# Kernel optimization log

Measured on AMD Instinct MI355X. Metric: run time of the kernel, lower is better.

Reference implementation:

```python
import jax, jax.numpy as jnp
import numpy as np

B, S, H, D, K = 262144, 120, 256, 64, 64  # batch, state_dim, vae_hidden_dim, latent_dim, n_codes


def _lin(k, i, o):
    return jax.random.normal(k, (i, o), jnp.float32) / np.sqrt(i).astype(np.float32)


def setup_inputs() -> dict:
    key = jax.random.key(0)
    ks = jax.random.split(key, 9)
    return {
        "inputs": jax.random.normal(ks[0], (B, S), jnp.float32),
        "enc_w1": _lin(ks[1], S, H), "enc_b1": jnp.zeros((H,), jnp.float32),
        "enc_w2": _lin(ks[2], H, H), "enc_b2": jnp.zeros((H,), jnp.float32),
        "enc_w3": _lin(ks[3], H, D), "enc_b3": jnp.zeros((D,), jnp.float32),
        "codebook": jax.random.uniform(ks[4], (K, D), jnp.float32),  # NearestEmbed weight (rand init)
        "fc3_w": _lin(ks[5], D, H), "fc3_b": jnp.zeros((H,), jnp.float32),
        "fc4_w": _lin(ks[6], H, H), "fc4_b": jnp.zeros((H,), jnp.float32),
        "fc5_w": _lin(ks[7], H, S), "fc5_b": jnp.zeros((S,), jnp.float32),
    }


def _nearest(z, codebook):
    # squared L2 distance via |z|^2 - 2 z.C^T + |c|^2; fused GEMM form
    d = ((z * z).sum(-1, keepdims=True)
         - 2.0 * (z @ codebook.T)
         + (codebook * codebook).sum(-1))  # [B, K]
    idx = jnp.argmin(d, axis=-1)  # [B]
    return codebook[idx], idx


def reference(inputs, enc_w1, enc_b1, enc_w2, enc_b2, enc_w3, enc_b3,
              codebook, fc3_w, fc3_b, fc4_w, fc4_b, fc5_w, fc5_b):
    # encode
    h = jax.nn.relu(inputs @ enc_w1 + enc_b1)
    h = jax.nn.relu(h @ enc_w2 + enc_b2)
    z_e = h @ enc_w3 + enc_b3  # [B, D]
    # emb(z_e, weight_sg=True): straight-through to input, codebook detached
    q, argmin = _nearest(z_e, jax.lax.stop_gradient(codebook))
    z_q = z_e + jax.lax.stop_gradient(q - z_e)
    # emb(z_e.detach()): grads flow only to codebook
    emb, _ = _nearest(jax.lax.stop_gradient(z_e), codebook)
    # decode (recon_type=1)
    r = jax.nn.relu(z_q @ fc3_w + fc3_b)
    r = jax.nn.relu(r @ fc4_w + fc4_b)
    s_hat = r @ fc5_w + fc5_b  # [B, S]
    return s_hat, z_e, emb, argmin
```

## Files before the change

kernel.cpp:

```cpp
#include <hip/hip_runtime.h>


#define B_TOTAL 262144
#define THR 0.02f

typedef float  f32x4 __attribute__((ext_vector_type(4)));
typedef short  s16x8 __attribute__((ext_vector_type(8)));

#define ZB ((size_t)B_TOTAL * 120)
#define EB ((size_t)B_TOTAL * 184)
#define AB ((size_t)B_TOTAL * 248)

#define WS_STAB   0
#define WS_CBT    30720
#define WS_CNORM  47104
#define WS_COUNT  47360
#define WS_LIST   47424
#define WS_PKW1   1096064
#define WS_PKW2   1227136
#define WS_PKE3   1489280
#define WS_PKW4   1554816
#define WS_CN2    1620352

static __device__ __forceinline__ unsigned short f2bf(float x) {
    unsigned int u = __float_as_uint(x);
    return (unsigned short)((u + 0x7fffu + ((u >> 16) & 1u)) >> 16);
}
static __device__ __forceinline__ void splitbf(float a, unsigned short& h, unsigned short& s) {
    unsigned hb = __float_as_uint(a) & 0xffff0000u;
    h = (unsigned short)(hb >> 16);
    s = f2bf(a - __uint_as_float(hb));
}
static __device__ __forceinline__ void splitbf_t(float a, unsigned short& h, unsigned short& s) {
    unsigned u = __float_as_uint(a);
    h = (unsigned short)(u >> 16);
    float d = a - __uint_as_float(u & 0xffff0000u);
    s = (unsigned short)(__float_as_uint(d) >> 16);
}
static __device__ __forceinline__ float sqnc(float v) {
    float s = v * v;
    asm volatile("" : "+v"(s));
    return s;
}
static __device__ __forceinline__ float np_sumsq64(const float* a) {
    float r8[8];
#pragma unroll
    for (int j = 0; j < 8; ++j) r8[j] = sqnc(a[j]);
#pragma unroll
    for (int i = 8; i < 64; i += 8)
#pragma unroll
        for (int j = 0; j < 8; ++j) r8[j] += sqnc(a[i + j]);
    return ((r8[0] + r8[1]) + (r8[2] + r8[3])) + ((r8[4] + r8[5]) + (r8[6] + r8[7]));
}

static __device__ __forceinline__ int swz(int row, int col) {
    return row * 256 + ((((col >> 3) ^ (row & 7))) << 3) + (col & 7);
}

__global__ __launch_bounds__(256)
void vq_prep(const float* __restrict__ cb,
             const float* __restrict__ dw3, const float* __restrict__ db3,
             const float* __restrict__ dw4, const float* __restrict__ db4,
             const float* __restrict__ dw5, const float* __restrict__ db5,
             float* __restrict__ s_tab, float* __restrict__ cbT, float* __restrict__ cnorm)
{
    __shared__ float c_row[64];
    __shared__ float u1[256];
    __shared__ float u2[256];
    const int k = blockIdx.x;
    const int t = threadIdx.x;

    if (t < 64) c_row[t] = cb[k * 64 + t];
    __syncthreads();
    {
        float s = 0.f;
        for (int f = 0; f < 64; ++f) s = fmaf(c_row[f], dw3[f * 256 + t], s);
        u1[t] = fmaxf(s + db3[t], 0.f);
    }
    if (t < 64) cbT[t * 64 + k] = c_row[t];
    if (t == 0) cnorm[k] = np_sumsq64(&cb[k * 64]);
    __syncthreads();
    {
        float s = 0.f;
        for (int f = 0; f < 256; ++f) s = fmaf(u1[f], dw4[f * 256 + t], s);
        u2[t] = fmaxf(s + db4[t], 0.f);
    }
    __syncthreads();
    if (t < 120) {
        float o = 0.f;
        for (int f = 0; f < 256; ++f) o = fmaf(u2[f], dw5[f * 120 + t], o);
        s_tab[k * 120 + t] = o + db5[t];
    }
}

__global__ __launch_bounds__(512)
void vq_pack(const float* __restrict__ w1, const float* __restrict__ w2,
             const float* __restrict__ ew3, const float* __restrict__ cb,
             const float* __restrict__ eb3,
             unsigned short* __restrict__ pw1, unsigned short* __restrict__ pw2,
             unsigned short* __restrict__ pe3, unsigned short* __restrict__ pw4,
             float* __restrict__ cn2, int* __restrict__ flag_count)
{
    const int t = threadIdx.x;
    int f = blockIdx.x;
    if (f == 0 && t == 0) *flag_count = 0;

    const int lane = t >> 3, j = t & 7;
    float a;
    unsigned short* dst;
    int nt, ks, KSN;

    if (f < 224) {
        const float* src; int srcK, ld;
        if (f < 64)       { src = w1;  dst = pw1; KSN = 4; nt = f >> 2;  ks = f & 3; srcK = 120; ld = 256; }
        else if (f < 192) { f -= 64;  src = w2;  dst = pw2; KSN = 8; nt = f >> 3; ks = f & 7; srcK = 256; ld = 256; }
        else              { f -= 192; src = ew3; dst = pe3; KSN = 8; nt = f >> 3; ks = f & 7; srcK = 256; ld = 64; }
        const int k = ks * 32 + (lane >> 4) * 8 + j;
        const int n = nt * 16 + (lane & 15);
        a = (k < srcK) ? src[k * ld + n] : 0.f;
    } else {
        int g = f - 224;
        dst = pw4; KSN = 8; nt = g >> 3; ks = g & 7;
        const int k = ks * 32 + (lane >> 4) * 8 + j;
        const int n = nt * 16 + (lane & 15);
        float s = 0.f;
        const float* er = ew3 + k * 64;
        const float* cr = cb + n * 64;
        for (int d = 0; d < 64; ++d) s = fmaf(er[d], cr[d], s);
        a = s;
        if (g == 0 && t < 64) {
            float ss = 0.f, e2 = 0.f;
            const float* c = cb + t * 64;
            for (int d = 0; d < 64; ++d) { ss = fmaf(c[d], c[d], ss); e2 = fmaf(eb3[d], c[d], e2); }
            cn2[t] = ss - 2.f * e2;
        }
    }

    unsigned short h, l;
    splitbf(a, h, l);
    const int base = (nt * KSN + ks) * 2 * 512;
    dst[base + t] = h;
    dst[base + 512 + t] = l;
}

__global__ __launch_bounds__(512, 4)
void vq_fast(const float* __restrict__ x,
             const float* __restrict__ b1, const float* __restrict__ b2,
             const float* __restrict__ eb3, const float* __restrict__ cb,
             const float* __restrict__ s_tab, const float* __restrict__ cn2,
             const unsigned short* __restrict__ pw1, const unsigned short* __restrict__ pw2,
             const unsigned short* __restrict__ pe3, const unsigned short* __restrict__ pw4,
             int* __restrict__ flag_count, int* __restrict__ flag_list,
             float* __restrict__ out)
{
    __shared__ __align__(16) unsigned char smem[32768];
    unsigned short* ph = (unsigned short*)smem;
    unsigned short* pl = (unsigned short*)(smem + 16384);
    float*          dm = (float*)smem;
    int*          idxs = (int*)(smem + 8704);

    const int t = threadIdx.x;
    const int w = t >> 6, l = t & 63;
    const int lr = l & 15;
    const int grow0 = blockIdx.x * 32;

    {
        const float* xb = x + (size_t)grow0 * 120;
        unsigned* ph32 = (unsigned*)ph;
        unsigned* pl32 = (unsigned*)pl;
#pragma unroll
        for (int i = 0; i < 4; ++i) {
            int p = t + 512 * i;
            if (p < 1920) {
                int row = p / 60, c2 = p - row * 60;
                float2 v = *(const float2*)&xb[row * 120 + c2 * 2];
                unsigned u0 = __float_as_uint(v.x);
                unsigned u1 = __float_as_uint(v.y);
                unsigned h0u = u0 & 0xffff0000u;
                unsigned h1u = u1 & 0xffff0000u;
                float d0 = v.x - __uint_as_float(h0u);
                float d1 = v.y - __uint_as_float(h1u);
                int o32 = row * 128 + ((((c2 >> 2) ^ (row & 7))) << 2) + (c2 & 3);
                ph32[o32] = (u0 >> 16) | h1u;
                pl32[o32] = (__float_as_uint(d0) >> 16) | (__float_as_uint(d1) & 0xffff0000u);
            }
        }
        if (t < 128) {
            int row = t >> 2, c2 = 60 + (t & 3);
            int o32 = row * 128 + ((((c2 >> 2) ^ (row & 7))) << 2) + (c2 & 3);
            ph32[o32] = 0u;
            pl32[o32] = 0u;
        }
    }
    __syncthreads();

    {
        f32x4 acc[2][2];
#pragma unroll
        for (int a = 0; a < 2; ++a)
#pragma unroll
            for (int b = 0; b < 2; ++b) acc[a][b] = (f32x4)0.f;

#pragma unroll
        for (int ks = 0; ks < 4; ++ks) {
            const int kb = ks * 32 + (l >> 4) * 8;
            s16x8 ah[2], al[2];
#pragma unroll
            for (int rt = 0; rt < 2; ++rt) {
                const int ro = swz(rt * 16 + lr, kb);
                ah[rt] = *(const s16x8*)&ph[ro];
                al[rt] = *(const s16x8*)&pl[ro];
            }
            s16x8 bh[2], bl[2];
#pragma unroll
            for (int ct = 0; ct < 2; ++ct) {
                const unsigned short* pb = pw1 + ((w * 2 + ct) * 4 + ks) * 1024 + l * 8;
                bh[ct] = *(const s16x8*)pb;
                bl[ct] = *(const s16x8*)(pb + 512);
            }
            __builtin_amdgcn_s_setprio(1);
#pragma unroll
            for (int ct = 0; ct < 2; ++ct)
#pragma unroll
                for (int rt = 0; rt < 2; ++rt) {
                    acc[rt][ct] = __builtin_amdgcn_mfma_f32_16x16x32_bf16(ah[rt], bh[ct], acc[rt][ct], 0, 0, 0);
                    acc[rt][ct] = __builtin_amdgcn_mfma_f32_16x16x32_bf16(ah[rt], bl[ct], acc[rt][ct], 0, 0, 0);
                    acc[rt][ct] = __builtin_amdgcn_mfma_f32_16x16x32_bf16(al[rt], bh[ct], acc[rt][ct], 0, 0, 0);
                }
            __builtin_amdgcn_s_setprio(0);
        }
        __syncthreads();
#pragma unroll
        for (int ct = 0; ct < 2; ++ct) {
            const int col = w * 32 + ct * 16 + lr;
            const float bb = b1[col];
#pragma unroll
            for (int rt = 0; rt < 2; ++rt)
#pragma unroll
                for (int r = 0; r < 4; ++r) {
                    float v = fmaxf(acc[rt][ct][r] + bb, 0.f);
                    unsigned short h, s;
                    splitbf_t(v, h, s);
                    const int row = rt * 16 + (l >> 4) * 4 + r;
                    const int o = swz(row, col);
                    ph[o] = h;
                    pl[o] = s;
                }
        }
    }
    __syncthreads();

    {
        f32x4 acc[2][2];
#pragma unroll
        for (int a = 0; a < 2; ++a)
#pragma unroll
            for (int b = 0; b < 2; ++b) acc[a][b] = (f32x4)0.f;

#pragma unroll
        for (int ks = 0; ks < 8; ++ks) {
            const int kb = ks * 32 + (l >> 4) * 8;
            s16x8 ah[2], al[2];
#pragma unroll
            for (int rt = 0; rt < 2; ++rt) {
                const int ro = swz(rt * 16 + lr, kb);
                ah[rt] = *(const s16x8*)&ph[ro];
                al[rt] = *(const s16x8*)&pl[ro];
            }
            s16x8 bh[2], bl[2];
#pragma unroll
            for (int ct = 0; ct < 2; ++ct) {
                const unsigned short* pb = pw2 + ((w * 2 + ct) * 8 + ks) * 1024 + l * 8;
                bh[ct] = *(const s16x8*)pb;
                bl[ct] = *(const s16x8*)(pb + 512);
            }
            __builtin_amdgcn_s_setprio(1);
#pragma unroll
            for (int ct = 0; ct < 2; ++ct)
#pragma unroll
                for (int rt = 0; rt < 2; ++rt) {
                    acc[rt][ct] = __builtin_amdgcn_mfma_f32_16x16x32_bf16(ah[rt], bh[ct], acc[rt][ct], 0, 0, 0);
                    acc[rt][ct] = __builtin_amdgcn_mfma_f32_16x16x32_bf16(ah[rt], bl[ct], acc[rt][ct], 0, 0, 0);
                    acc[rt][ct] = __builtin_amdgcn_mfma_f32_16x16x32_bf16(al[rt], bh[ct], acc[rt][ct], 0, 0, 0);
                }
            __builtin_amdgcn_s_setprio(0);
        }
        __syncthreads();
#pragma unroll
        for (int ct = 0; ct < 2; ++ct) {
            const int col = w * 32 + ct * 16 + lr;
            const float bb = b2[col];
#pragma unroll
            for (int rt = 0; rt < 2; ++rt)
#pragma unroll
                for (int r = 0; r < 4; ++r) {
                    float v = fmaxf(acc[rt][ct][r] + bb, 0.f);
                    unsigned short h, s;
                    splitbf_t(v, h, s);
                    const int row = rt * 16 + (l >> 4) * 4 + r;
                    const int o = swz(row, col);
                    ph[o] = h;
                    pl[o] = s;
                }
        }
    }
    __syncthreads();

    const int wrow = w & 1, wcol = w >> 1;
    const int rA = wrow * 16 + lr;
    {
        f32x4 a3 = (f32x4)0.f;
        f32x4 a4 = (f32x4)0.f;

#pragma unroll
        for (int ks = 0; ks < 8; ++ks) {
            const int kb = ks * 32 + (l >> 4) * 8;
            const int ro = swz(rA, kb);
            s16x8 ah = *(const s16x8*)&ph[ro];
            s16x8 al = *(const s16x8*)&pl[ro];
            const unsigned short* pb3 = pe3 + (wcol * 8 + ks) * 1024 + l * 8;
            const unsigned short* pb4 = pw4 + (wcol * 8 + ks) * 1024 + l * 8;
            s16x8 bh3 = *(const s16x8*)pb3;
            s16x8 bl3 = *(const s16x8*)(pb3 + 512);
            s16x8 bh4 = *(const s16x8*)pb4;
            s16x8 bl4 = *(const s16x8*)(pb4 + 512);
            __builtin_amdgcn_s_setprio(1);
            a3 = __builtin_amdgcn_mfma_f32_16x16x32_bf16(ah, bh3, a3, 0, 0, 0);
            a3 = __builtin_amdgcn_mfma_f32_16x16x32_bf16(ah, bl3, a3, 0, 0, 0);
            a3 = __builtin_amdgcn_mfma_f32_16x16x32_bf16(al, bh3, a3, 0, 0, 0);
            a4 = __builtin_amdgcn_mfma_f32_16x16x32_bf16(ah, bh4, a4, 0, 0, 0);
            a4 = __builtin_amdgcn_mfma_f32_16x16x32_bf16(ah, bl4, a4, 0, 0, 0);
            a4 = __builtin_amdgcn_mfma_f32_16x16x32_bf16(al, bh4, a4, 0, 0, 0);
            __builtin_amdgcn_s_setprio(0);
        }
        __syncthreads();

        const int col = wcol * 16 + lr;
        const float eb = eb3[col];
        const float cn = cn2[col];
#pragma unroll
        for (int r = 0; r < 4; ++r) {
            const int row = wrow * 16 + (l >> 4) * 4 + r;
            out[ZB + (size_t)(grow0 + row) * 64 + col] = a3[r] + eb;
            dm[row * 68 + col] = cn - 2.f * a4[r];
        }
    }
    __syncthreads();

    if (t < 32) {
        const float* dr = dm + t * 68;
        float best = dr[0], sec = 3.4e38f;
        int bi = 0;
        for (int j = 1; j < 64; ++j) {
            float v = dr[j];
            if (v < best) { sec = best; best = v; bi = j; }
            else if (v < sec) sec = v;
        }
        idxs[t] = bi;
        out[AB + grow0 + t] = (float)bi;
        if (sec - best < THR) {
            int p = atomicAdd(flag_count, 1);
            if (p < B_TOTAL) flag_list[p] = grow0 + t;
        }
    }
    __syncthreads();

#pragma unroll
    for (int i = 0; i < 4; ++i) {
        int p = t + 512 * i;
        int row = p >> 6, c = p & 63;
        out[EB + (size_t)blockIdx.x * 2048 + p] = cb[idxs[row] * 64 + c];
    }
#pragma unroll
    for (int i = 0; i < 8; ++i) {
        int p = t + 512 * i;
        if (p < 3840) {
            int row = p / 120, c = p - row * 120;
            out[(size_t)blockIdx.x * 3840 + p] = s_tab[idxs[row] * 120 + c];
        }
    }
}

__global__ __launch_bounds__(256)
void vq_exact(const float* __restrict__ x,
              const float* __restrict__ w1, const float* __restrict__ b1,
              const float* __restrict__ w2, const float* __restrict__ b2,
              const float* __restrict__ ew3, const float* __restrict__ eb3,
              const float* __restrict__ cb,
              const float* __restrict__ s_tab,
              const float* __restrict__ cbT, const float* __restrict__ cnorm,
              const int* __restrict__ flag_count, const int* __restrict__ flag_list,
              float* __restrict__ out)
{
    __shared__ float act[256 * 18];
    __shared__ float zrm[16 * 68];
    __shared__ float dmr[16 * 68];
    __shared__ float A_lds[16];
    __shared__ int   idxs[16];
    __shared__ int   rl[16];

    const int t = threadIdx.x;
    int count = *flag_count;
    if (count > B_TOTAL) count = B_TOTAL;

    const int tx = t & 31;
    const int ty = t >> 5;
    const int r0 = ty * 2;
    const int c0 = tx * 8;
    const int c0d = tx * 2;

    for (int base = blockIdx.x * 16; base < count; base += 1024 * 16) {
        if (t < 16) {
            int li = base + t;
            rl[t] = flag_list[li < count ? li : count - 1];
        }
        __syncthreads();

        for (int i = 0; i < 8; ++i) {
            int p = t + 256 * i;
            if (p < 1920) {
                int r = p / 120;
                int c = p - r * 120;
                act[c * 18 + r] = x[(size_t)rl[r] * 120 + c];
            }
        }
        __syncthreads();

        {
            float acc[2][8];
#pragma unroll
            for (int i = 0; i < 2; ++i)
#pragma unroll
                for (int c = 0; c < 8; ++c) acc[i][c] = 0.f;
#pragma unroll 2
            for (int k = 0; k < 120; ++k) {
                const float2 av = *(const float2*)&act[k * 18 + r0];
                const float4 wv0 = *(const float4*)&w1[k * 256 + c0];
                const float4 wv1 = *(const float4*)&w1[k * 256 + c0 + 4];
                const float a[2] = {av.x, av.y};
                const float wv[8] = {wv0.x, wv0.y, wv0.z, wv0.w, wv1.x, wv1.y, wv1.z, wv1.w};
#pragma unroll
                for (int i = 0; i < 2; ++i)
#pragma unroll
                    for (int c = 0; c < 8; ++c) acc[i][c] = fmaf(a[i], wv[c], acc[i][c]);
            }
            __syncthreads();
            const float4 bv0 = *(const float4*)&b1[c0];
            const float4 bv1 = *(const float4*)&b1[c0 + 4];
            const float bb[8] = {bv0.x, bv0.y, bv0.z, bv0.w, bv1.x, bv1.y, bv1.z, bv1.w};
#pragma unroll
            for (int c = 0; c < 8; ++c)
#pragma unroll
                for (int i = 0; i < 2; ++i)
                    act[(c0 + c) * 18 + r0 + i] = fmaxf(acc[i][c] + bb[c], 0.f);
        }
        __syncthreads();

        {
            float acc[2][8];
#pragma unroll
            for (int i = 0; i < 2; ++i)
#pragma unroll
                for (int c = 0; c < 8; ++c) acc[i][c] = 0.f;
#pragma unroll 2
            for (int k = 0; k < 256; ++k) {
                const float2 av = *(const float2*)&act[k * 18 + r0];
                const float4 wv0 = *(const float4*)&w2[k * 256 + c0];
                const float4 wv1 = *(const float4*)&w2[k * 256 + c0 + 4];
                const float a[2] = {av.x, av.y};
                const float wv[8] = {wv0.x, wv0.y, wv0.z, wv0.w, wv1.x, wv1.y, wv1.z, wv1.w};
#pragma unroll
                for (int i = 0; i < 2; ++i)
#pragma unroll
                    for (int c = 0; c < 8; ++c) acc[i][c] = fmaf(a[i], wv[c], acc[i][c]);
            }
            __syncthreads();
            const float4 bv0 = *(const float4*)&b2[c0];
            const float4 bv1 = *(const float4*)&b2[c0 + 4];
            const float bb[8] = {bv0.x, bv0.y, bv0.z, bv0.w, bv1.x, bv1.y, bv1.z, bv1.w};
#pragma unroll
            for (int c = 0; c < 8; ++c)
#pragma unroll
                for (int i = 0; i < 2; ++i)
                    act[(c0 + c) * 18 + r0 + i] = fmaxf(acc[i][c] + bb[c], 0.f);
        }
        __syncthreads();

        {
            float acc2[2][2];
#pragma unroll
            for (int i = 0; i < 2; ++i) { acc2[i][0] = 0.f; acc2[i][1] = 0.f; }
#pragma unroll 2
            for (int k = 0; k < 256; ++k) {
                const float2 av = *(const float2*)&act[k * 18 + r0];
                const float2 wv = *(const float2*)&ew3[k * 64 + c0d];
#pragma unroll
                for (int i = 0; i < 2; ++i) {
                    float a = (i == 0) ? av.x : av.y;
                    acc2[i][0] = fmaf(a, wv.x, acc2[i][0]);
                    acc2[i][1] = fmaf(a, wv.y, acc2[i][1]);
                }
            }
            __syncthreads();
            const float2 bv = *(const float2*)&eb3[c0d];
#pragma unroll
            for (int i = 0; i < 2; ++i) {
                float z0 = acc2[i][0] + bv.x;
                float z1 = acc2[i][1] + bv.y;
                act[(c0d + 0) * 18 + r0 + i] = z0;
                act[(c0d + 1) * 18 + r0 + i] = z1;
                zrm[(r0 + i) * 68 + c0d]     = z0;
                zrm[(r0 + i) * 68 + c0d + 1] = z1;
            }
        }
        __syncthreads();

        if (t < 16) A_lds[t] = np_sumsq64(&zrm[t * 68]);
        __syncthreads();

        {
            float acc3[2][2];
#pragma unroll
            for (int i = 0; i < 2; ++i) { acc3[i][0] = 0.f; acc3[i][1] = 0.f; }
#pragma unroll 2
            for (int k = 0; k < 64; ++k) {
                const float2 av = *(const float2*)&act[k * 18 + r0];
                const float2 wv = *(const float2*)&cbT[k * 64 + c0d];
#pragma unroll
                for (int i = 0; i < 2; ++i) {
                    float a = (i == 0) ? av.x : av.y;
                    acc3[i][0] = fmaf(a, wv.x, acc3[i][0]);
                    acc3[i][1] = fmaf(a, wv.y, acc3[i][1]);
                }
            }
            const float cn0 = cnorm[c0d], cn1 = cnorm[c0d + 1];
#pragma unroll
            for (int i = 0; i < 2; ++i) {
                float g0 = 2.0f * acc3[i][0];  asm volatile("" : "+v"(g0));
                float g1 = 2.0f * acc3[i][1];  asm volatile("" : "+v"(g1));
                const float Ar = A_lds[r0 + i];
                dmr[(r0 + i) * 68 + c0d]     = (Ar - g0) + cn0;
                dmr[(r0 + i) * 68 + c0d + 1] = (Ar - g1) + cn1;
            }
        }
        __syncthreads();

        if (t < 16) {
            const float* dr = &dmr[t * 68];
            float best = dr[0];
            int bi = 0;
            for (int c = 1; c < 64; ++c) {
                float v = dr[c];
                if (v < best) { best = v; bi = c; }
            }
            idxs[t] = bi;
            out[AB + rl[t]] = (float)bi;
        }
        __syncthreads();

        {
            const int r = t >> 4, q = t & 15;
            *(float4*)(out + ZB + (size_t)rl[r] * 64 + q * 4) = *(const float4*)&zrm[r * 68 + q * 4];
        }
        {
            const int r = t >> 4, q = t & 15;
            *(float4*)(out + EB + (size_t)rl[r] * 64 + q * 4) = *(const float4*)(cb + idxs[r] * 64 + q * 4);
        }
        for (int i = 0; i < 8; ++i) {
            int p = t + 256 * i;
            if (p < 1920) {
                int r = p / 120;
                int c = p - r * 120;
                out[(size_t)rl[r] * 120 + c] = s_tab[idxs[r] * 120 + c];
            }
        }
        __syncthreads();
    }
}

extern "C" void kernel_launch(void* const* d_in, const int* in_sizes, int n_in,
                              void* d_out, int out_size, void* d_ws, size_t ws_size,
                              hipStream_t stream)
{
    const float* x   = (const float*)d_in[0];
    const float* w1  = (const float*)d_in[1];
    const float* b1  = (const float*)d_in[2];
    const float* w2  = (const float*)d_in[3];
    const float* b2  = (const float*)d_in[4];
    const float* ew3 = (const float*)d_in[5];
    const float* eb3 = (const float*)d_in[6];
    const float* cb  = (const float*)d_in[7];
    const float* dw3 = (const float*)d_in[8];
    const float* db3 = (const float*)d_in[9];
    const float* dw4 = (const float*)d_in[10];
    const float* db4 = (const float*)d_in[11];
    const float* dw5 = (const float*)d_in[12];
    const float* db5 = (const float*)d_in[13];

    float* out = (float*)d_out;
    char* ws = (char*)d_ws;
    float* s_tab = (float*)(ws + WS_STAB);
    float* cbT   = (float*)(ws + WS_CBT);
    float* cnorm = (float*)(ws + WS_CNORM);
    int*   fcnt  = (int*)(ws + WS_COUNT);
    int*   flist = (int*)(ws + WS_LIST);
    unsigned short* pw1 = (unsigned short*)(ws + WS_PKW1);
    unsigned short* pw2 = (unsigned short*)(ws + WS_PKW2);
    unsigned short* pe3 = (unsigned short*)(ws + WS_PKE3);
    unsigned short* pw4 = (unsigned short*)(ws + WS_PKW4);
    float* cn2 = (float*)(ws + WS_CN2);

    vq_prep<<<64, 256, 0, stream>>>(cb, dw3, db3, dw4, db4, dw5, db5,
                                    s_tab, cbT, cnorm);
    vq_pack<<<256, 512, 0, stream>>>(w1, w2, ew3, cb, eb3,
                                     pw1, pw2, pe3, pw4, cn2, fcnt);
    vq_fast<<<B_TOTAL / 32, 512, 0, stream>>>(x, b1, b2, eb3, cb, s_tab, cn2,
                                              pw1, pw2, pe3, pw4, fcnt, flist, out);
    vq_exact<<<1024, 256, 0, stream>>>(x, w1, b1, w2, b2, ew3, eb3, cb,
                                       s_tab, cbT, cnorm, fcnt, flist, out);
}
```

Before: 494.1 us.

## Process 64 rows per block to reuse weight fragments across more row tiles

Doubles the batch tile per workgroup from 32 to 64 rows, so each wave loads weight fragments once and applies them to four row tiles instead of two. The final stage assigns half the waves to the encoder output projection and half to the codebook distance projection, instead of each wave doing both. This halves weight fragment traffic and block count. In exchange it doubles LDS to 64KB per block and increases accumulator registers, which lowers achievable occupancy.

```diff
diff --git a/kernel.cpp b/kernel.cpp
--- a/kernel.cpp
+++ b/kernel.cpp
@@ -153,25 +153,25 @@
              int* __restrict__ flag_count, int* __restrict__ flag_list,
              float* __restrict__ out)
 {
-    __shared__ __align__(16) unsigned char smem[32768];
+    __shared__ __align__(16) unsigned char smem[65536];
     unsigned short* ph = (unsigned short*)smem;
-    unsigned short* pl = (unsigned short*)(smem + 16384);
+    unsigned short* pl = (unsigned short*)(smem + 32768);
     float*          dm = (float*)smem;
-    int*          idxs = (int*)(smem + 8704);
+    int*          idxs = (int*)(smem + 17408);
 
     const int t = threadIdx.x;
     const int w = t >> 6, l = t & 63;
     const int lr = l & 15;
-    const int grow0 = blockIdx.x * 32;
+    const int grow0 = blockIdx.x * 64;
 
     {
         const float* xb = x + (size_t)grow0 * 120;
         unsigned* ph32 = (unsigned*)ph;
         unsigned* pl32 = (unsigned*)pl;
 #pragma unroll
-        for (int i = 0; i < 4; ++i) {
+        for (int i = 0; i < 8; ++i) {
             int p = t + 512 * i;
-            if (p < 1920) {
+            if (p < 3840) {
                 int row = p / 60, c2 = p - row * 60;
                 float2 v = *(const float2*)&xb[row * 120 + c2 * 2];
                 unsigned u0 = __float_as_uint(v.x);
@@ -185,7 +185,7 @@
                 pl32[o32] = (__float_as_uint(d0) >> 16) | (__float_as_uint(d1) & 0xffff0000u);
             }
         }
-        if (t < 128) {
+        if (t < 256) {
             int row = t >> 2, c2 = 60 + (t & 3);
             int o32 = row * 128 + ((((c2 >> 2) ^ (row & 7))) << 2) + (c2 & 3);
             ph32[o32] = 0u;
@@ -195,22 +195,15 @@
     __syncthreads();
 
     {
-        f32x4 acc[2][2];
-#pragma unroll
-        for (int a = 0; a < 2; ++a)
+        f32x4 acc[4][2];
+#pragma unroll
+        for (int a = 0; a < 4; ++a)
 #pragma unroll
             for (int b = 0; b < 2; ++b) acc[a][b] = (f32x4)0.f;
 
 #pragma unroll
         for (int ks = 0; ks < 4; ++ks) {
             const int kb = ks * 32 + (l >> 4) * 8;
-            s16x8 ah[2], al[2];
-#pragma unroll
-            for (int rt = 0; rt < 2; ++rt) {
-                const int ro = swz(rt * 16 + lr, kb);
-                ah[rt] = *(const s16x8*)&ph[ro];
-                al[rt] = *(const s16x8*)&pl[ro];
-            }
             s16x8 bh[2], bl[2];
 #pragma unroll
             for (int ct = 0; ct < 2; ++ct) {
@@ -218,16 +211,20 @@
                 bh[ct] = *(const s16x8*)pb;
                 bl[ct] = *(const s16x8*)(pb + 512);
             }
-            __builtin_amdgcn_s_setprio(1);
-#pragma unroll
-            for (int ct = 0; ct < 2; ++ct)
-#pragma unroll
-                for (int rt = 0; rt < 2; ++rt) {
-                    acc[rt][ct] = __builtin_amdgcn_mfma_f32_16x16x32_bf16(ah[rt], bh[ct], acc[rt][ct], 0, 0, 0);
-                    acc[rt][ct] = __builtin_amdgcn_mfma_f32_16x16x32_bf16(ah[rt], bl[ct], acc[rt][ct], 0, 0, 0);
-                    acc[rt][ct] = __builtin_amdgcn_mfma_f32_16x16x32_bf16(al[rt], bh[ct], acc[rt][ct], 0, 0, 0);
-                }
-            __builtin_amdgcn_s_setprio(0);
+#pragma unroll
+            for (int rt = 0; rt < 4; ++rt) {
+                const int ro = swz(rt * 16 + lr, kb);
+                s16x8 ah = *(const s16x8*)&ph[ro];
+                s16x8 al = *(const s16x8*)&pl[ro];
+                __builtin_amdgcn_s_setprio(1);
+#pragma unroll
+                for (int ct = 0; ct < 2; ++ct) {
+                    acc[rt][ct] = __builtin_amdgcn_mfma_f32_16x16x32_bf16(ah, bh[ct], acc[rt][ct], 0, 0, 0);
+                    acc[rt][ct] = __builtin_amdgcn_mfma_f32_16x16x32_bf16(ah, bl[ct], acc[rt][ct], 0, 0, 0);
+                    acc[rt][ct] = __builtin_amdgcn_mfma_f32_16x16x32_bf16(al, bh[ct], acc[rt][ct], 0, 0, 0);
+                }
+                __builtin_amdgcn_s_setprio(0);
+            }
         }
         __syncthreads();
 #pragma unroll
@@ -235,7 +232,7 @@
             const int col = w * 32 + ct * 16 + lr;
             const float bb = b1[col];
 #pragma unroll
-            for (int rt = 0; rt < 2; ++rt)
+            for (int rt = 0; rt < 4; ++rt)
 #pragma unroll
                 for (int r = 0; r < 4; ++r) {
                     float v = fmaxf(acc[rt][ct][r] + bb, 0.f);
@@ -251,22 +248,15 @@
     __syncthreads();
 
     {
-        f32x4 acc[2][2];
-#pragma unroll
-        for (int a = 0; a < 2; ++a)
+        f32x4 acc[4][2];
+#pragma unroll
+        for (int a = 0; a < 4; ++a)
 #pragma unroll
             for (int b = 0; b < 2; ++b) acc[a][b] = (f32x4)0.f;
 
 #pragma unroll
         for (int ks = 0; ks < 8; ++ks) {
             const int kb = ks * 32 + (l >> 4) * 8;
-            s16x8 ah[2], al[2];
-#pragma unroll
-            for (int rt = 0; rt < 2; ++rt) {
-                const int ro = swz(rt * 16 + lr, kb);
-                ah[rt] = *(const s16x8*)&ph[ro];
-                al[rt] = *(const s16x8*)&pl[ro];
-            }
             s16x8 bh[2], bl[2];
 #pragma unroll
             for (int ct = 0; ct < 2; ++ct) {
@@ -274,16 +264,20 @@
                 bh[ct] = *(const s16x8*)pb;
                 bl[ct] = *(const s16x8*)(pb + 512);
             }
-            __builtin_amdgcn_s_setprio(1);
-#pragma unroll
-            for (int ct = 0; ct < 2; ++ct)
-#pragma unroll
-                for (int rt = 0; rt < 2; ++rt) {
-                    acc[rt][ct] = __builtin_amdgcn_mfma_f32_16x16x32_bf16(ah[rt], bh[ct], acc[rt][ct], 0, 0, 0);
-                    acc[rt][ct] = __builtin_amdgcn_mfma_f32_16x16x32_bf16(ah[rt], bl[ct], acc[rt][ct], 0, 0, 0);
-                    acc[rt][ct] = __builtin_amdgcn_mfma_f32_16x16x32_bf16(al[rt], bh[ct], acc[rt][ct], 0, 0, 0);
-                }
-            __builtin_amdgcn_s_setprio(0);
+#pragma unroll
+            for (int rt = 0; rt < 4; ++rt) {
+                const int ro = swz(rt * 16 + lr, kb);
+                s16x8 ah = *(const s16x8*)&ph[ro];
+                s16x8 al = *(const s16x8*)&pl[ro];
+                __builtin_amdgcn_s_setprio(1);
+#pragma unroll
+                for (int ct = 0; ct < 2; ++ct) {
+                    acc[rt][ct] = __builtin_amdgcn_mfma_f32_16x16x32_bf16(ah, bh[ct], acc[rt][ct], 0, 0, 0);
+                    acc[rt][ct] = __builtin_amdgcn_mfma_f32_16x16x32_bf16(ah, bl[ct], acc[rt][ct], 0, 0, 0);
+                    acc[rt][ct] = __builtin_amdgcn_mfma_f32_16x16x32_bf16(al, bh[ct], acc[rt][ct], 0, 0, 0);
+                }
+                __builtin_amdgcn_s_setprio(0);
+            }
         }
         __syncthreads();
 #pragma unroll
@@ -291,7 +285,7 @@
             const int col = w * 32 + ct * 16 + lr;
             const float bb = b2[col];
 #pragma unroll
-            for (int rt = 0; rt < 2; ++rt)
+            for (int rt = 0; rt < 4; ++rt)
 #pragma unroll
                 for (int r = 0; r < 4; ++r) {
                     float v = fmaxf(acc[rt][ct][r] + bb, 0.f);
@@ -306,48 +300,58 @@
     }
     __syncthreads();
 
-    const int wrow = w & 1, wcol = w >> 1;
-    const int rA = wrow * 16 + lr;
+    const int mat = w >> 2;
+    const int ct3 = w & 3;
     {
-        f32x4 a3 = (f32x4)0.f;
-        f32x4 a4 = (f32x4)0.f;
+        f32x4 a[4];
+#pragma unroll
+        for (int rt = 0; rt < 4; ++rt) a[rt] = (f32x4)0.f;
+        const unsigned short* pmat = mat ? pw4 : pe3;
 
 #pragma unroll
         for (int ks = 0; ks < 8; ++ks) {
             const int kb = ks * 32 + (l >> 4) * 8;
-            const int ro = swz(rA, kb);
-            s16x8 ah = *(const s16x8*)&ph[ro];
-            s16x8 al = *(const s16x8*)&pl[ro];
-            const unsigned short* pb3 = pe3 + (wcol * 8 + ks) * 1024 + l * 8;
-            const unsigned short* pb4 = pw4 + (wcol * 8 + ks) * 1024 + l * 8;
-            s16x8 bh3 = *(const s16x8*)pb3;
-            s16x8 bl3 = *(const s16x8*)(pb3 + 512);
-            s16x8 bh4 = *(const s16x8*)pb4;
-            s16x8 bl4 = *(const s16x8*)(pb4 + 512);
-            __builtin_amdgcn_s_setprio(1);
-            a3 = __builtin_amdgcn_mfma_f32_16x16x32_bf16(ah, bh3, a3, 0, 0, 0);
-            a3 = __builtin_amdgcn_mfma_f32_16x16x32_bf16(ah, bl3, a3, 0, 0, 0);
-            a3 = __builtin_amdgcn_mfma_f32_16x16x32_bf16(al, bh3, a3, 0, 0, 0);
-            a4 = __builtin_amdgcn_mfma_f32_16x16x32_bf16(ah, bh4, a4, 0, 0, 0);
-            a4 = __builtin_amdgcn_mfma_f32_16x16x32_bf16(ah, bl4, a4, 0, 0, 0);
-            a4 = __builtin_amdgcn_mfma_f32_16x16x32_bf16(al, bh4, a4, 0, 0, 0);
-            __builtin_amdgcn_s_setprio(0);
-        }
-        __syncthreads();
-
-        const int col = wcol * 16 + lr;
-        const float eb = eb3[col];
-        const float cn = cn2[col];
-#pragma unroll
-        for (int r = 0; r < 4; ++r) {
-            const int row = wrow * 16 + (l >> 4) * 4 + r;
-            out[ZB + (size_t)(grow0 + row) * 64 + col] = a3[r] + eb;
-            dm[row * 68 + col] = cn - 2.f * a4[r];
-        }
-    }
-    __syncthreads();
-
-    if (t < 32) {
+            const unsigned short* pb = pmat + (ct3 * 8 + ks) * 1024 + l * 8;
+            s16x8 bh = *(const s16x8*)pb;
+            s16x8 bl = *(const s16x8*)(pb + 512);
+#pragma unroll
+            for (int rt = 0; rt < 4; ++rt) {
+                const int ro = swz(rt * 16 + lr, kb);
+                s16x8 ah = *(const s16x8*)&ph[ro];
+                s16x8 al = *(const s16x8*)&pl[ro];
+                __builtin_amdgcn_s_setprio(1);
+                a[rt] = __builtin_amdgcn_mfma_f32_16x16x32_bf16(ah, bh, a[rt], 0, 0, 0);
+                a[rt] = __builtin_amdgcn_mfma_f32_16x16x32_bf16(ah, bl, a[rt], 0, 0, 0);
+                a[rt] = __builtin_amdgcn_mfma_f32_16x16x32_bf16(al, bh, a[rt], 0, 0, 0);
+                __builtin_amdgcn_s_setprio(0);
+            }
+        }
+        __syncthreads();
+
+        const int col = ct3 * 16 + lr;
+        if (mat == 0) {
+            const float eb = eb3[col];
+#pragma unroll
+            for (int rt = 0; rt < 4; ++rt)
+#pragma unroll
+                for (int r = 0; r < 4; ++r) {
+                    const int row = rt * 16 + (l >> 4) * 4 + r;
+                    out[ZB + (size_t)(grow0 + row) * 64 + col] = a[rt][r] + eb;
+                }
+        } else {
+            const float cn = cn2[col];
+#pragma unroll
+            for (int rt = 0; rt < 4; ++rt)
+#pragma unroll
+                for (int r = 0; r < 4; ++r) {
+                    const int row = rt * 16 + (l >> 4) * 4 + r;
+                    dm[row * 68 + col] = cn - 2.f * a[rt][r];
+                }
+        }
+    }
+    __syncthreads();
+
+    if (t < 64) {
         const float* dr = dm + t * 68;
         float best = dr[0], sec = 3.4e38f;
         int bi = 0;
@@ -366,18 +370,16 @@
     __syncthreads();
 
 #pragma unroll
-    for (int i = 0; i < 4; ++i) {
+    for (int i = 0; i < 8; ++i) {
         int p = t + 512 * i;
         int row = p >> 6, c = p & 63;
-        out[EB + (size_t)blockIdx.x * 2048 + p] = cb[idxs[row] * 64 + c];
-    }
-#pragma unroll
-    for (int i = 0; i < 8; ++i) {
+        out[EB + (size_t)blockIdx.x * 4096 + p] = cb[idxs[row] * 64 + c];
+    }
+#pragma unroll
+    for (int i = 0; i < 15; ++i) {
         int p = t + 512 * i;
-        if (p < 3840) {
-            int row = p / 120, c = p - row * 120;
-            out[(size_t)blockIdx.x * 3840 + p] = s_tab[idxs[row] * 120 + c];
-        }
+        int row = p / 120, c = p - row * 120;
+        out[(size_t)blockIdx.x * 7680 + p] = s_tab[idxs[row] * 120 + c];
     }
 }
 
@@ -614,7 +616,7 @@
                                     s_tab, cbT, cnorm);
     vq_pack<<<256, 512, 0, stream>>>(w1, w2, ew3, cb, eb3,
                                      pw1, pw2, pe3, pw4, cn2, fcnt);
-    vq_fast<<<B_TOTAL / 32, 512, 0, stream>>>(x, b1, b2, eb3, cb, s_tab, cn2,
+    vq_fast<<<B_TOTAL / 64, 512, 0, stream>>>(x, b1, b2, eb3, cb, s_tab, cn2,
                                               pw1, pw2, pe3, pw4, fcnt, flist, out);
     vq_exact<<<1024, 256, 0, stream>>>(x, w1, b1, w2, b2, ew3, eb3, cb,
                                        s_tab, cbT, cnorm, fcnt, flist, out);
```

Result: faster. 429.8 us (-13.0%).
